# Optimization experiments

Hardware: AMD Instinct MI355X
Metric: run time of the kernel (lower is better)

## Reference

```python
import jax, jax.numpy as jnp
import numpy as np

N = 200000          # nodes
E = 6400000         # edges (avg degree 32)
IN_C, HID, OUT_C = 128, 16, 2


def gcn_conv(x, W, b, src, dst, n):
    """PyG GCNConv: out = D^{-1/2} (A + I) D^{-1/2} (x W) + b."""
    h = x @ W  # transform first (in_channels >= out_channels): [n, d_out]
    loop = jnp.arange(n)
    s = jnp.concatenate([src, loop])  # add self-loops
    d = jnp.concatenate([dst, loop])
    ew = jnp.ones(s.shape[0], x.dtype)
    deg = jax.ops.segment_sum(ew, d, num_segments=n)  # in-degree incl. self-loop
    dinv = jnp.where(deg > 0, jax.lax.rsqrt(deg), jnp.zeros((), x.dtype))
    norm = dinv[s] * dinv[d]                          # [E+n]
    msg = h[s] * norm[:, None]                        # gather + scale
    out = jax.ops.segment_sum(msg, d, num_segments=n) # scatter-add
    return out + b


def setup_inputs() -> dict:
    key = jax.random.key(0)
    k1, k2, k3, k4 = jax.random.split(key, 4)
    x = jax.random.normal(k1, (N, IN_C), dtype=jnp.float32)
    edge_index = jax.random.randint(k2, (2, E), 0, N, dtype=jnp.int64)
    # Glorot-style init like PyG GCNConv
    W1 = jax.random.normal(k3, (IN_C, HID), dtype=jnp.float32) * (1.0 / np.sqrt(IN_C))
    b1 = jnp.zeros((HID,), jnp.float32)
    W2 = jax.random.normal(k4, (HID, OUT_C), dtype=jnp.float32) * (1.0 / np.sqrt(HID))
    b2 = jnp.zeros((OUT_C,), jnp.float32)
    return {"x": x, "edge_index": edge_index, "W1": W1, "b1": b1, "W2": W2, "b2": b2}


def reference(x, edge_index, W1, b1, W2, b2):
    src, dst = edge_index[0], edge_index[1]
    h = gcn_conv(x, W1, b1, src, dst, N)
    h = jax.nn.relu(h)
    return gcn_conv(h, W2, b2, src, dst, N)
```

## Files before the change

### kernel.cpp

```cpp
#include <hip/hip_runtime.h>
#include <hip/hip_fp16.h>

#define NN   200000
#define EE   6400000
#define INC  128
#define HIDC 16
#define OUTC 2

#define TN     256
#define TSHIFT 8
#define TMASK  (TN - 1)
#define NT     782
#define CHUNK  8192
#define NBE    782
#define SCAP   9216
#define QSH    15
#define NQ     8

__global__ __launch_bounds__(1024) void k_init(int* __restrict__ gcur) {
    int t = threadIdx.x;
    if (t < NT) gcur[t] = t * SCAP;
}

__global__ __launch_bounds__(256) void k_place(const int* __restrict__ src,
                                               const int* __restrict__ dst,
                                               int* __restrict__ gcur,
                                               int* __restrict__ brec) {
    __shared__ int h[NT];
    __shared__ int lbase[NT];
    __shared__ int gofs[NT];
    __shared__ int stmp[256];
    __shared__ int lrec[CHUNK];
    __shared__ unsigned short ltid[CHUNK];

    int tid = threadIdx.x;
    int base = blockIdx.x * CHUNK;
    int nrec = EE - base; if (nrec > CHUNK) nrec = CHUNK;
    bool full = (base + CHUNK <= EE);

    for (int t = tid; t < NT; t += 256) h[t] = 0;
    __syncthreads();
    if (full) {
        for (int i = tid; i < CHUNK; i += 1024) {
            int d0 = dst[base + i];
            int d1 = dst[base + i + 256];
            int d2 = dst[base + i + 512];
            int d3 = dst[base + i + 768];
            atomicAdd(&h[d0 >> TSHIFT], 1);
            atomicAdd(&h[d1 >> TSHIFT], 1);
            atomicAdd(&h[d2 >> TSHIFT], 1);
            atomicAdd(&h[d3 >> TSHIFT], 1);
        }
    } else {
        for (int i = tid; i < nrec; i += 256)
            atomicAdd(&h[dst[base + i] >> TSHIFT], 1);
    }
    __syncthreads();

    int t0 = tid * 4;
    int c0 = (t0 + 0 < NT) ? h[t0 + 0] : 0;
    int c1 = (t0 + 1 < NT) ? h[t0 + 1] : 0;
    int c2 = (t0 + 2 < NT) ? h[t0 + 2] : 0;
    int c3 = (t0 + 3 < NT) ? h[t0 + 3] : 0;
    int s = c0 + c1 + c2 + c3;
    stmp[tid] = s;
    __syncthreads();
    for (int o = 1; o < 256; o <<= 1) {
        int u = (tid >= o) ? stmp[tid - o] : 0;
        __syncthreads();
        stmp[tid] += u;
        __syncthreads();
    }
    int run = stmp[tid] - s;
    if (t0 + 0 < NT) { lbase[t0 + 0] = run; run += c0; }
    if (t0 + 1 < NT) { lbase[t0 + 1] = run; run += c1; }
    if (t0 + 2 < NT) { lbase[t0 + 2] = run; run += c2; }
    if (t0 + 3 < NT) { lbase[t0 + 3] = run; run += c3; }
    __syncthreads();

    for (int t = tid; t < NT; t += 256) {
        int c = h[t];
        int gb = c ? atomicAdd(&gcur[t], c) : 0;
        gofs[t] = gb - lbase[t];
    }
    __syncthreads();

    if (full) {
        for (int i = tid; i < CHUNK; i += 1024) {
            int e = base + i;
            int d0 = dst[e], d1 = dst[e + 256], d2 = dst[e + 512], d3 = dst[e + 768];
            int s0 = src[e], s1 = src[e + 256], s2 = src[e + 512], s3 = src[e + 768];
            int t0_ = d0 >> TSHIFT, t1_ = d1 >> TSHIFT;
            int t2_ = d2 >> TSHIFT, t3_ = d3 >> TSHIFT;
            int p0 = atomicAdd(&lbase[t0_], 1);
            int p1 = atomicAdd(&lbase[t1_], 1);
            int p2 = atomicAdd(&lbase[t2_], 1);
            int p3 = atomicAdd(&lbase[t3_], 1);
            lrec[p0] = (s0 << 8) | (d0 & TMASK); ltid[p0] = (unsigned short)t0_;
            lrec[p1] = (s1 << 8) | (d1 & TMASK); ltid[p1] = (unsigned short)t1_;
            lrec[p2] = (s2 << 8) | (d2 & TMASK); ltid[p2] = (unsigned short)t2_;
            lrec[p3] = (s3 << 8) | (d3 & TMASK); ltid[p3] = (unsigned short)t3_;
        }
    } else {
        for (int i = tid; i < nrec; i += 256) {
            int e = base + i;
            int d = dst[e], ss = src[e];
            int tt = d >> TSHIFT;
            int p = atomicAdd(&lbase[tt], 1);
            lrec[p] = (ss << 8) | (d & TMASK); ltid[p] = (unsigned short)tt;
        }
    }
    __syncthreads();

    for (int i = tid; i < nrec; i += 256) {
        int r = lrec[i];
        int tt = ltid[i];
        brec[gofs[tt] + i] = r;
    }
}

__global__ __launch_bounds__(256) void k_sortt(int* __restrict__ brec,
                                               const int* __restrict__ gcur,
                                               int* __restrict__ nstart,
                                               int* __restrict__ ndeg) {
    __shared__ int rec[SCAP];
    __shared__ int h[TN * NQ];
    __shared__ int cur[TN * NQ];
    __shared__ int stmp[256];
    int t = blockIdx.x;
    int s0 = t * SCAP;
    int cnt = gcur[t] - s0;
    if (cnt > SCAP) cnt = SCAP;
    int tid = threadIdx.x;
    for (int k = tid; k < TN * NQ; k += 256) h[k] = 0;
    __syncthreads();
    for (int i = tid; i < cnt; i += 256) {
        int r = brec[s0 + i];
        rec[i] = r;
        unsigned q = (unsigned)(r >> 8) >> QSH;
        atomicAdd(&h[((unsigned)(r & TMASK) << 3) | q], 1);
    }
    __syncthreads();
    int k0 = tid * NQ;
    int s = 0;
#pragma unroll
    for (int j = 0; j < NQ; ++j) s += h[k0 + j];
    stmp[tid] = s;
    __syncthreads();
    for (int o = 1; o < 256; o <<= 1) {
        int u = (tid >= o) ? stmp[tid - o] : 0;
        __syncthreads();
        stmp[tid] += u;
        __syncthreads();
    }
    int run = stmp[tid] - s;
    int node = t * TN + tid;
    if (node < NN) {
        nstart[node] = s0 + run;
        ndeg[node] = s;
    }
#pragma unroll
    for (int j = 0; j < NQ; ++j) {
        cur[k0 + j] = run;
        run += h[k0 + j];
    }
    __syncthreads();
    for (int i = tid; i < cnt; i += 256) {
        int r = rec[i];
        unsigned q = (unsigned)(r >> 8) >> QSH;
        int pos = atomicAdd(&cur[((unsigned)(r & TMASK) << 3) | q], 1);
        brec[s0 + pos] = r >> 8;
    }
}

__global__ __launch_bounds__(256) void k_xw(const float* __restrict__ x,
                                            const float* __restrict__ W1,
                                            const int* __restrict__ ndeg,
                                            __half2* __restrict__ g1) {
    __shared__ float Ws[INC * HIDC];
    for (int j = threadIdx.x; j < INC * HIDC; j += 256) Ws[j] = W1[j];
    __syncthreads();
    int n = blockIdx.x * 256 + threadIdx.x;
    if (n >= NN) return;
    const float4* xr = (const float4*)(x + (size_t)n * INC);
    float acc[HIDC];
#pragma unroll
    for (int c = 0; c < HIDC; ++c) acc[c] = 0.f;
    for (int k4 = 0; k4 < INC / 4; ++k4) {
        float4 xv = xr[k4];
        const float* w0 = &Ws[(k4 * 4) * HIDC];
        float xs[4] = {xv.x, xv.y, xv.z, xv.w};
#pragma unroll
        for (int j = 0; j < 4; ++j) {
#pragma unroll
            for (int c = 0; c < HIDC; ++c) acc[c] += xs[j] * w0[j * HIDC + c];
        }
    }
    float dn = rsqrtf((float)(ndeg[n] + 1));
    union { __half2 h[8]; float4 f[2]; } u;
#pragma unroll
    for (int q = 0; q < 8; ++q)
        u.h[q] = __floats2half2_rn(dn * acc[2 * q], dn * acc[2 * q + 1]);
    float4* gp = (float4*)(g1 + (size_t)n * 8);
    gp[0] = u.f[0];
    gp[1] = u.f[1];
}

__global__ __launch_bounds__(256) void k_agg1n(const int* __restrict__ csr,
                                               const int* __restrict__ nstart,
                                               const int* __restrict__ ndeg,
                                               const __half2* __restrict__ g1,
                                               const float* __restrict__ b1,
                                               const float* __restrict__ W2,
                                               float* __restrict__ g2) {
    int lane = threadIdx.x & 7;
    int n = (blockIdx.x * 256 + threadIdx.x) >> 3;
    if (n >= NN) return;
    int rs = nstart[n];
    int deg = ndeg[n];
    int re = rs + deg;
    float dn = rsqrtf((float)(deg + 1));
    float2 s = __half22float2(g1[(size_t)n * 8 + lane]);
    float ax = s.x, ay = s.y;
    int i = rs;
    for (; i + 4 <= re; i += 4) {
        int s0 = csr[i], s1 = csr[i + 1], s2 = csr[i + 2], s3 = csr[i + 3];
        float2 f0 = __half22float2(g1[(size_t)s0 * 8 + lane]);
        float2 f1 = __half22float2(g1[(size_t)s1 * 8 + lane]);
        float2 f2 = __half22float2(g1[(size_t)s2 * 8 + lane]);
        float2 f3 = __half22float2(g1[(size_t)s3 * 8 + lane]);
        ax += f0.x + f1.x + f2.x + f3.x;
        ay += f0.y + f1.y + f2.y + f3.y;
    }
    for (; i < re; ++i) {
        float2 f = __half22float2(g1[(size_t)csr[i] * 8 + lane]);
        ax += f.x; ay += f.y;
    }
    float h0 = fmaxf(fmaf(dn, ax, b1[2 * lane]), 0.f);
    float h1 = fmaxf(fmaf(dn, ay, b1[2 * lane + 1]), 0.f);
    float p0 = h0 * W2[(2 * lane) * OUTC + 0] + h1 * W2[(2 * lane + 1) * OUTC + 0];
    float p1 = h0 * W2[(2 * lane) * OUTC + 1] + h1 * W2[(2 * lane + 1) * OUTC + 1];
#pragma unroll
    for (int o = 4; o; o >>= 1) {
        p0 += __shfl_xor(p0, o, 8);
        p1 += __shfl_xor(p1, o, 8);
    }
    if (lane == 0) {
        float2 v; v.x = dn * p0; v.y = dn * p1;
        ((float2*)g2)[n] = v;
    }
}

__global__ __launch_bounds__(256) void k_agg2n(const int* __restrict__ csr,
                                               const int* __restrict__ nstart,
                                               const int* __restrict__ ndeg,
                                               const float* __restrict__ g2,
                                               const float* __restrict__ b2,
                                               float* __restrict__ out) {
    int lane = threadIdx.x & 7;
    int n = (blockIdx.x * 256 + threadIdx.x) >> 3;
    if (n >= NN) return;
    int rs = nstart[n];
    int deg = ndeg[n];
    int re = rs + deg;
    float dn = rsqrtf((float)(deg + 1));
    float ax = 0.f, ay = 0.f;
    for (int i = rs + lane; i < re; i += 8) {
        float2 v = ((const float2*)g2)[csr[i]];
        ax += v.x; ay += v.y;
    }
#pragma unroll
    for (int o = 4; o; o >>= 1) {
        ax += __shfl_xor(ax, o, 8);
        ay += __shfl_xor(ay, o, 8);
    }
    if (lane == 0) {
        float2 g = ((const float2*)g2)[n];
        float2 o2;
        o2.x = fmaf(dn, ax + g.x, b2[0]);
        o2.y = fmaf(dn, ay + g.y, b2[1]);
        ((float2*)out)[n] = o2;
    }
}


__global__ void k_deg_f(const int* __restrict__ dst, int* __restrict__ deg) {
    int i = blockIdx.x * blockDim.x + threadIdx.x;
    if (i < EE) atomicAdd(&deg[dst[i]], 1);
}
__global__ void k_dinv_f(const int* __restrict__ deg, float* __restrict__ dinv) {
    int n = blockIdx.x * blockDim.x + threadIdx.x;
    if (n < NN) dinv[n] = rsqrtf((float)(deg[n] + 1));
}
__global__ void k_xw_f(const float* __restrict__ x, const float* __restrict__ W1,
                       const float* __restrict__ dinv, float* __restrict__ g1) {
    __shared__ float Ws[INC * HIDC];
    for (int j = threadIdx.x; j < INC * HIDC; j += 256) Ws[j] = W1[j];
    __syncthreads();
    int n = blockIdx.x * 256 + threadIdx.x;
    if (n >= NN) return;
    const float4* xr = (const float4*)(x + (size_t)n * INC);
    float acc[HIDC];
#pragma unroll
    for (int c = 0; c < HIDC; ++c) acc[c] = 0.f;
    for (int k4 = 0; k4 < INC / 4; ++k4) {
        float4 xv = xr[k4];
        const float* w0 = &Ws[(k4 * 4) * HIDC];
        float xs[4] = {xv.x, xv.y, xv.z, xv.w};
#pragma unroll
        for (int j = 0; j < 4; ++j)
#pragma unroll
            for (int c = 0; c < HIDC; ++c) acc[c] += xs[j] * w0[j * HIDC + c];
    }
    float dn = dinv[n];
#pragma unroll
    for (int c = 0; c < HIDC; ++c) g1[(size_t)n * HIDC + c] = dn * acc[c];
}
__global__ void k_scatter1_f(const int* __restrict__ src, const int* __restrict__ dst,
                             const float* __restrict__ g1, float* __restrict__ acc1) {
    int i = blockIdx.x * blockDim.x + threadIdx.x;
    if (i >= EE * 4) return;
    int e = i >> 2, q = i & 3;
    float4 v = ((const float4*)g1)[src[e] * 4 + q];
    float* p = acc1 + (size_t)dst[e] * HIDC + q * 4;
    unsafeAtomicAdd(p + 0, v.x); unsafeAtomicAdd(p + 1, v.y);
    unsafeAtomicAdd(p + 2, v.z); unsafeAtomicAdd(p + 3, v.w);
}
__global__ void k_l2_f(const float* __restrict__ g1, const float* __restrict__ acc1,
                       const float* __restrict__ dinv, const float* __restrict__ b1,
                       const float* __restrict__ W2, float* __restrict__ g2) {
    int n = blockIdx.x * blockDim.x + threadIdx.x;
    if (n >= NN) return;
    float dn = dinv[n];
    float h[HIDC];
#pragma unroll
    for (int c = 0; c < HIDC; ++c)
        h[c] = fmaxf(dn * (acc1[(size_t)n * HIDC + c] + g1[(size_t)n * HIDC + c]) + b1[c], 0.f);
    float o0 = 0.f, o1 = 0.f;
#pragma unroll
    for (int c = 0; c < HIDC; ++c) { o0 += h[c] * W2[c * 2]; o1 += h[c] * W2[c * 2 + 1]; }
    g2[(size_t)n * 2] = dn * o0; g2[(size_t)n * 2 + 1] = dn * o1;
}
__global__ void k_scatter2_f(const int* __restrict__ src, const int* __restrict__ dst,
                             const float* __restrict__ g2, float* __restrict__ acc2) {
    int e = blockIdx.x * blockDim.x + threadIdx.x;
    if (e >= EE) return;
    float2 v = ((const float2*)g2)[src[e]];
    unsafeAtomicAdd(&acc2[(size_t)dst[e] * 2], v.x);
    unsafeAtomicAdd(&acc2[(size_t)dst[e] * 2 + 1], v.y);
}
__global__ void k_final_f(const float* __restrict__ g2, const float* __restrict__ acc2,
                          const float* __restrict__ dinv, const float* __restrict__ b2,
                          float* __restrict__ out) {
    int n = blockIdx.x * blockDim.x + threadIdx.x;
    if (n >= NN) return;
    float dn = dinv[n];
    float2 a = ((const float2*)acc2)[n];
    float2 g = ((const float2*)g2)[n];
    float2 o;
    o.x = dn * (a.x + g.x) + b2[0];
    o.y = dn * (a.y + g.y) + b2[1];
    ((float2*)out)[n] = o;
}


extern "C" void kernel_launch(void* const* d_in, const int* in_sizes, int n_in,
                              void* d_out, int out_size, void* d_ws, size_t ws_size,
                              hipStream_t stream) {
    const float* x  = (const float*)d_in[0];
    const int*   ei = (const int*)d_in[1];
    const float* W1 = (const float*)d_in[2];
    const float* b1 = (const float*)d_in[3];
    const float* W2 = (const float*)d_in[4];
    const float* b2 = (const float*)d_in[5];
    float* out = (float*)d_out;

    const int* src = ei;
    const int* dst = ei + EE;
    const int B = 256;

    size_t need = ((size_t)NT + (size_t)NT * SCAP + (size_t)(NN + 1) + (size_t)NN +
                   (size_t)8 * NN + (size_t)2 * NN) * 4;
    if (ws_size >= need) {
        int* ws          = (int*)d_ws;
        int* gcur        = ws;
        int* brec        = ws + NT;
        int* nstart      = brec + (size_t)NT * SCAP;
        int* ndeg        = nstart + NN + 1;
        __half2* g1      = (__half2*)(ndeg + NN);
        float* g2        = (float*)((int*)(ndeg + NN) + (size_t)8 * NN);

        k_init  <<<1, 1024, 0, stream>>>(gcur);
        k_place <<<NBE, 256, 0, stream>>>(src, dst, gcur, brec);
        k_sortt <<<NT, 256, 0, stream>>>(brec, gcur, nstart, ndeg);
        k_xw    <<<(NN + 255) / 256, 256, 0, stream>>>(x, W1, ndeg, g1);
        k_agg1n <<<(NN * 8 + 255) / 256, 256, 0, stream>>>(brec, nstart, ndeg, g1, b1, W2, g2);
        k_agg2n <<<(NN * 8 + 255) / 256, 256, 0, stream>>>(brec, nstart, ndeg, g2, b2, out);
        return;
    }

    char* wsb = (char*)d_ws;
    int*   deg  = (int*)wsb;
    float* acc1 = (float*)(wsb + (size_t)NN * 4);
    float* acc2 = (float*)(wsb + (size_t)17 * NN * 4);
    float* dinv = (float*)(wsb + (size_t)19 * NN * 4);
    float* g1   = (float*)(wsb + (size_t)20 * NN * 4);
    float* g2   = (float*)(wsb + (size_t)36 * NN * 4);

    hipMemsetAsync(d_ws, 0, (size_t)19 * NN * 4, stream);

    int gN = (NN + B - 1) / B, gE = (EE + B - 1) / B, gE4 = (EE * 4 + B - 1) / B;
    k_deg_f     <<<gE, B, 0, stream>>>(dst, deg);
    k_dinv_f    <<<gN, B, 0, stream>>>(deg, dinv);
    k_xw_f      <<<gN, B, 0, stream>>>(x, W1, dinv, g1);
    k_scatter1_f<<<gE4, B, 0, stream>>>(src, dst, g1, acc1);
    k_l2_f      <<<gN, B, 0, stream>>>(g1, acc1, dinv, b1, W2, g2);
    k_scatter2_f<<<gE, B, 0, stream>>>(src, dst, g2, acc2);
    k_final_f   <<<gN, B, 0, stream>>>(g2, acc2, dinv, b2, out);
}
```

Before: 407.1 us.

## Replace per-node CSR aggregation with per-tile LDS atomic accumulation

The sort kernel now orders records within each 256-node tile by source-range bucket first and then by destination, keeping the packed record instead of building per-node CSR offsets. Both aggregation kernels now run one block per tile, sweeping that tile's records and accumulating into shared-memory arrays with LDS float atomics rather than walking each node's neighbor list. This removes the nstart array and the uneven per-node loops, and the source-bucket order is meant to improve gather locality. The cost is heavy LDS atomic traffic (16 atomics per edge in layer one) and a floating-point summation order that now varies between runs.

```diff
diff --git a/kernel.cpp b/kernel.cpp
--- a/kernel.cpp
+++ b/kernel.cpp
@@ -121,7 +121,6 @@
 
 __global__ __launch_bounds__(256) void k_sortt(int* __restrict__ brec,
                                                const int* __restrict__ gcur,
-                                               int* __restrict__ nstart,
                                                int* __restrict__ ndeg) {
     __shared__ int rec[SCAP];
     __shared__ int h[TN * NQ];
@@ -137,14 +136,19 @@
     for (int i = tid; i < cnt; i += 256) {
         int r = brec[s0 + i];
         rec[i] = r;
-        unsigned q = (unsigned)(r >> 8) >> QSH;
-        atomicAdd(&h[((unsigned)(r & TMASK) << 3) | q], 1);
-    }
-    __syncthreads();
-    int k0 = tid * NQ;
+        unsigned key = (((unsigned)r >> (8 + QSH)) << 8) | ((unsigned)r & TMASK);
+        atomicAdd(&h[key], 1);
+    }
+    __syncthreads();
+    int node = t * TN + tid;
+    int dsum = 0;
+#pragma unroll
+    for (int q = 0; q < NQ; ++q) dsum += h[(q << 8) | tid];
+    if (node < NN) ndeg[node] = dsum;
+    int k0 = tid * 8;
     int s = 0;
 #pragma unroll
-    for (int j = 0; j < NQ; ++j) s += h[k0 + j];
+    for (int j = 0; j < 8; ++j) s += h[k0 + j];
     stmp[tid] = s;
     __syncthreads();
     for (int o = 1; o < 256; o <<= 1) {
@@ -154,22 +158,14 @@
         __syncthreads();
     }
     int run = stmp[tid] - s;
-    int node = t * TN + tid;
-    if (node < NN) {
-        nstart[node] = s0 + run;
-        ndeg[node] = s;
-    }
-#pragma unroll
-    for (int j = 0; j < NQ; ++j) {
-        cur[k0 + j] = run;
-        run += h[k0 + j];
-    }
+#pragma unroll
+    for (int j = 0; j < 8; ++j) { cur[k0 + j] = run; run += h[k0 + j]; }
     __syncthreads();
     for (int i = tid; i < cnt; i += 256) {
         int r = rec[i];
-        unsigned q = (unsigned)(r >> 8) >> QSH;
-        int pos = atomicAdd(&cur[((unsigned)(r & TMASK) << 3) | q], 1);
-        brec[s0 + pos] = r >> 8;
+        unsigned key = (((unsigned)r >> (8 + QSH)) << 8) | ((unsigned)r & TMASK);
+        int pos = atomicAdd(&cur[key], 1);
+        brec[s0 + pos] = r;
     }
 }
 
@@ -206,79 +202,117 @@
     gp[1] = u.f[1];
 }
 
-__global__ __launch_bounds__(256) void k_agg1n(const int* __restrict__ csr,
-                                               const int* __restrict__ nstart,
+__global__ __launch_bounds__(256) void k_agg1t(const int* __restrict__ brec,
+                                               const int* __restrict__ gcur,
                                                const int* __restrict__ ndeg,
-                                               const __half2* __restrict__ g1,
+                                               const float4* __restrict__ g1,
                                                const float* __restrict__ b1,
                                                const float* __restrict__ W2,
                                                float* __restrict__ g2) {
-    int lane = threadIdx.x & 7;
-    int n = (blockIdx.x * 256 + threadIdx.x) >> 3;
-    if (n >= NN) return;
-    int rs = nstart[n];
-    int deg = ndeg[n];
-    int re = rs + deg;
-    float dn = rsqrtf((float)(deg + 1));
-    float2 s = __half22float2(g1[(size_t)n * 8 + lane]);
-    float ax = s.x, ay = s.y;
-    int i = rs;
-    for (; i + 4 <= re; i += 4) {
-        int s0 = csr[i], s1 = csr[i + 1], s2 = csr[i + 2], s3 = csr[i + 3];
-        float2 f0 = __half22float2(g1[(size_t)s0 * 8 + lane]);
-        float2 f1 = __half22float2(g1[(size_t)s1 * 8 + lane]);
-        float2 f2 = __half22float2(g1[(size_t)s2 * 8 + lane]);
-        float2 f3 = __half22float2(g1[(size_t)s3 * 8 + lane]);
-        ax += f0.x + f1.x + f2.x + f3.x;
-        ay += f0.y + f1.y + f2.y + f3.y;
-    }
-    for (; i < re; ++i) {
-        float2 f = __half22float2(g1[(size_t)csr[i] * 8 + lane]);
-        ax += f.x; ay += f.y;
-    }
-    float h0 = fmaxf(fmaf(dn, ax, b1[2 * lane]), 0.f);
-    float h1 = fmaxf(fmaf(dn, ay, b1[2 * lane + 1]), 0.f);
-    float p0 = h0 * W2[(2 * lane) * OUTC + 0] + h1 * W2[(2 * lane + 1) * OUTC + 0];
-    float p1 = h0 * W2[(2 * lane) * OUTC + 1] + h1 * W2[(2 * lane + 1) * OUTC + 1];
-#pragma unroll
-    for (int o = 4; o; o >>= 1) {
-        p0 += __shfl_xor(p0, o, 8);
-        p1 += __shfl_xor(p1, o, 8);
-    }
-    if (lane == 0) {
+    __shared__ float acc[HIDC][TN];
+    int t = blockIdx.x;
+    int tid = threadIdx.x;
+    int n = t * TN + tid;
+    union { float4 f[2]; __half2 h[8]; } us;
+    if (n < NN) { us.f[0] = g1[(size_t)n * 2]; us.f[1] = g1[(size_t)n * 2 + 1]; }
+    else        { us.f[0] = make_float4(0.f, 0.f, 0.f, 0.f);
+                  us.f[1] = make_float4(0.f, 0.f, 0.f, 0.f); }
+#pragma unroll
+    for (int q = 0; q < 8; ++q) {
+        float2 f = __half22float2(us.h[q]);
+        acc[2 * q][tid] = f.x;
+        acc[2 * q + 1][tid] = f.y;
+    }
+    __syncthreads();
+    int s0 = t * SCAP;
+    int cnt = gcur[t] - s0;
+    if (cnt > SCAP) cnt = SCAP;
+    int i = tid;
+    for (; i + 256 < cnt; i += 512) {
+        int r0 = brec[s0 + i];
+        int r1 = brec[s0 + i + 256];
+        int sA = r0 >> 8, dA = r0 & TMASK;
+        int sB = r1 >> 8, dB = r1 & TMASK;
+        union { float4 f[2]; __half2 h[8]; } uA, uB;
+        uA.f[0] = g1[(size_t)sA * 2]; uA.f[1] = g1[(size_t)sA * 2 + 1];
+        uB.f[0] = g1[(size_t)sB * 2]; uB.f[1] = g1[(size_t)sB * 2 + 1];
+#pragma unroll
+        for (int q = 0; q < 8; ++q) {
+            float2 fA = __half22float2(uA.h[q]);
+            float2 fB = __half22float2(uB.h[q]);
+            atomicAdd(&acc[2 * q][dA], fA.x);
+            atomicAdd(&acc[2 * q][dB], fB.x);
+            atomicAdd(&acc[2 * q + 1][dA], fA.y);
+            atomicAdd(&acc[2 * q + 1][dB], fB.y);
+        }
+    }
+    if (i < cnt) {
+        int r = brec[s0 + i];
+        int sA = r >> 8, dA = r & TMASK;
+        union { float4 f[2]; __half2 h[8]; } uA;
+        uA.f[0] = g1[(size_t)sA * 2]; uA.f[1] = g1[(size_t)sA * 2 + 1];
+#pragma unroll
+        for (int q = 0; q < 8; ++q) {
+            float2 f = __half22float2(uA.h[q]);
+            atomicAdd(&acc[2 * q][dA], f.x);
+            atomicAdd(&acc[2 * q + 1][dA], f.y);
+        }
+    }
+    __syncthreads();
+    if (n < NN) {
+        float dn = rsqrtf((float)(ndeg[n] + 1));
+        float p0 = 0.f, p1 = 0.f;
+#pragma unroll
+        for (int c = 0; c < HIDC; ++c) {
+            float hv = fmaxf(fmaf(dn, acc[c][tid], b1[c]), 0.f);
+            p0 = fmaf(hv, W2[c * OUTC + 0], p0);
+            p1 = fmaf(hv, W2[c * OUTC + 1], p1);
+        }
         float2 v; v.x = dn * p0; v.y = dn * p1;
         ((float2*)g2)[n] = v;
     }
 }
 
-__global__ __launch_bounds__(256) void k_agg2n(const int* __restrict__ csr,
-                                               const int* __restrict__ nstart,
+__global__ __launch_bounds__(256) void k_agg2t(const int* __restrict__ brec,
+                                               const int* __restrict__ gcur,
                                                const int* __restrict__ ndeg,
                                                const float* __restrict__ g2,
                                                const float* __restrict__ b2,
                                                float* __restrict__ out) {
-    int lane = threadIdx.x & 7;
-    int n = (blockIdx.x * 256 + threadIdx.x) >> 3;
-    if (n >= NN) return;
-    int rs = nstart[n];
-    int deg = ndeg[n];
-    int re = rs + deg;
-    float dn = rsqrtf((float)(deg + 1));
-    float ax = 0.f, ay = 0.f;
-    for (int i = rs + lane; i < re; i += 8) {
-        float2 v = ((const float2*)g2)[csr[i]];
-        ax += v.x; ay += v.y;
-    }
-#pragma unroll
-    for (int o = 4; o; o >>= 1) {
-        ax += __shfl_xor(ax, o, 8);
-        ay += __shfl_xor(ay, o, 8);
-    }
-    if (lane == 0) {
+    __shared__ float ax[TN];
+    __shared__ float ay[TN];
+    int t = blockIdx.x;
+    int tid = threadIdx.x;
+    ax[tid] = 0.f; ay[tid] = 0.f;
+    __syncthreads();
+    int s0 = t * SCAP;
+    int cnt = gcur[t] - s0;
+    if (cnt > SCAP) cnt = SCAP;
+    int i = tid;
+    for (; i + 256 < cnt; i += 512) {
+        int r0 = brec[s0 + i];
+        int r1 = brec[s0 + i + 256];
+        float2 v0 = ((const float2*)g2)[r0 >> 8];
+        float2 v1 = ((const float2*)g2)[r1 >> 8];
+        atomicAdd(&ax[r0 & TMASK], v0.x);
+        atomicAdd(&ax[r1 & TMASK], v1.x);
+        atomicAdd(&ay[r0 & TMASK], v0.y);
+        atomicAdd(&ay[r1 & TMASK], v1.y);
+    }
+    if (i < cnt) {
+        int r = brec[s0 + i];
+        float2 v = ((const float2*)g2)[r >> 8];
+        atomicAdd(&ax[r & TMASK], v.x);
+        atomicAdd(&ay[r & TMASK], v.y);
+    }
+    __syncthreads();
+    int n = t * TN + tid;
+    if (n < NN) {
+        float dn = rsqrtf((float)(ndeg[n] + 1));
         float2 g = ((const float2*)g2)[n];
         float2 o2;
-        o2.x = fmaf(dn, ax + g.x, b2[0]);
-        o2.y = fmaf(dn, ay + g.y, b2[1]);
+        o2.x = fmaf(dn, ax[tid] + g.x, b2[0]);
+        o2.y = fmaf(dn, ay[tid] + g.y, b2[1]);
         ((float2*)out)[n] = o2;
     }
 }
@@ -379,23 +413,22 @@
     const int* dst = ei + EE;
     const int B = 256;
 
-    size_t need = ((size_t)NT + (size_t)NT * SCAP + (size_t)(NN + 1) + (size_t)NN +
+    size_t need = ((size_t)NT + (size_t)NT * SCAP + (size_t)NN +
                    (size_t)8 * NN + (size_t)2 * NN) * 4;
     if (ws_size >= need) {
         int* ws          = (int*)d_ws;
         int* gcur        = ws;
         int* brec        = ws + NT;
-        int* nstart      = brec + (size_t)NT * SCAP;
-        int* ndeg        = nstart + NN + 1;
+        int* ndeg        = brec + (size_t)NT * SCAP;
         __half2* g1      = (__half2*)(ndeg + NN);
         float* g2        = (float*)((int*)(ndeg + NN) + (size_t)8 * NN);
 
         k_init  <<<1, 1024, 0, stream>>>(gcur);
         k_place <<<NBE, 256, 0, stream>>>(src, dst, gcur, brec);
-        k_sortt <<<NT, 256, 0, stream>>>(brec, gcur, nstart, ndeg);
+        k_sortt <<<NT, 256, 0, stream>>>(brec, gcur, ndeg);
         k_xw    <<<(NN + 255) / 256, 256, 0, stream>>>(x, W1, ndeg, g1);
-        k_agg1n <<<(NN * 8 + 255) / 256, 256, 0, stream>>>(brec, nstart, ndeg, g1, b1, W2, g2);
-        k_agg2n <<<(NN * 8 + 255) / 256, 256, 0, stream>>>(brec, nstart, ndeg, g2, b2, out);
+        k_agg1t <<<NT, 256, 0, stream>>>(brec, gcur, ndeg, (const float4*)g1, b1, W2, g2);
+        k_agg2t <<<NT, 256, 0, stream>>>(brec, gcur, ndeg, g2, b2, out);
         return;
     }
 
```

Measured after the change: 1.255 ms. +208.3%, slower.

## Switch aggregation kernels from 8-lanes-per-node to one thread per node

Applied to the files above, without the earlier changes.

Both aggregation kernels now assign one thread per destination node instead of an 8-lane group. Each thread loads whole 32-byte fp16 feature rows as two float4 loads per neighbour and accumulates all 16 channels in registers, which removes the cross-lane shuffle reductions. The intent is to cut shuffle overhead and issue fewer, wider gathers. In exchange, edge loops become serial per thread, the CSR index loads are no longer coalesced across lanes, degree imbalance within a wavefront causes divergence, and the 200k-thread grid offers far less parallelism to hide gather latency.

```diff
diff --git a/kernel.cpp b/kernel.cpp
--- a/kernel.cpp
+++ b/kernel.cpp
@@ -206,81 +206,94 @@
     gp[1] = u.f[1];
 }
 
-__global__ __launch_bounds__(256) void k_agg1n(const int* __restrict__ csr,
+__global__ __launch_bounds__(256) void k_agg1p(const int* __restrict__ csr,
                                                const int* __restrict__ nstart,
                                                const int* __restrict__ ndeg,
-                                               const __half2* __restrict__ g1,
+                                               const float4* __restrict__ g1,
                                                const float* __restrict__ b1,
                                                const float* __restrict__ W2,
                                                float* __restrict__ g2) {
-    int lane = threadIdx.x & 7;
-    int n = (blockIdx.x * 256 + threadIdx.x) >> 3;
+    int n = blockIdx.x * 256 + threadIdx.x;
     if (n >= NN) return;
     int rs = nstart[n];
     int deg = ndeg[n];
     int re = rs + deg;
     float dn = rsqrtf((float)(deg + 1));
-    float2 s = __half22float2(g1[(size_t)n * 8 + lane]);
-    float ax = s.x, ay = s.y;
+    float acc[HIDC];
+    {
+        union { float4 f[2]; __half2 h[8]; } u;
+        u.f[0] = g1[(size_t)n * 2]; u.f[1] = g1[(size_t)n * 2 + 1];
+#pragma unroll
+        for (int q = 0; q < 8; ++q) {
+            float2 f = __half22float2(u.h[q]);
+            acc[2 * q] = f.x; acc[2 * q + 1] = f.y;
+        }
+    }
     int i = rs;
-    for (; i + 4 <= re; i += 4) {
-        int s0 = csr[i], s1 = csr[i + 1], s2 = csr[i + 2], s3 = csr[i + 3];
-        float2 f0 = __half22float2(g1[(size_t)s0 * 8 + lane]);
-        float2 f1 = __half22float2(g1[(size_t)s1 * 8 + lane]);
-        float2 f2 = __half22float2(g1[(size_t)s2 * 8 + lane]);
-        float2 f3 = __half22float2(g1[(size_t)s3 * 8 + lane]);
-        ax += f0.x + f1.x + f2.x + f3.x;
-        ay += f0.y + f1.y + f2.y + f3.y;
-    }
-    for (; i < re; ++i) {
-        float2 f = __half22float2(g1[(size_t)csr[i] * 8 + lane]);
-        ax += f.x; ay += f.y;
-    }
-    float h0 = fmaxf(fmaf(dn, ax, b1[2 * lane]), 0.f);
-    float h1 = fmaxf(fmaf(dn, ay, b1[2 * lane + 1]), 0.f);
-    float p0 = h0 * W2[(2 * lane) * OUTC + 0] + h1 * W2[(2 * lane + 1) * OUTC + 0];
-    float p1 = h0 * W2[(2 * lane) * OUTC + 1] + h1 * W2[(2 * lane + 1) * OUTC + 1];
-#pragma unroll
-    for (int o = 4; o; o >>= 1) {
-        p0 += __shfl_xor(p0, o, 8);
-        p1 += __shfl_xor(p1, o, 8);
-    }
-    if (lane == 0) {
-        float2 v; v.x = dn * p0; v.y = dn * p1;
-        ((float2*)g2)[n] = v;
-    }
-}
-
-__global__ __launch_bounds__(256) void k_agg2n(const int* __restrict__ csr,
+    for (; i + 2 <= re; i += 2) {
+        int s0 = csr[i], s1 = csr[i + 1];
+        union { float4 f[2]; __half2 h[8]; } uA, uB;
+        uA.f[0] = g1[(size_t)s0 * 2]; uA.f[1] = g1[(size_t)s0 * 2 + 1];
+        uB.f[0] = g1[(size_t)s1 * 2]; uB.f[1] = g1[(size_t)s1 * 2 + 1];
+#pragma unroll
+        for (int q = 0; q < 8; ++q) {
+            float2 fA = __half22float2(uA.h[q]);
+            float2 fB = __half22float2(uB.h[q]);
+            acc[2 * q]     += fA.x + fB.x;
+            acc[2 * q + 1] += fA.y + fB.y;
+        }
+    }
+    if (i < re) {
+        int s0 = csr[i];
+        union { float4 f[2]; __half2 h[8]; } uA;
+        uA.f[0] = g1[(size_t)s0 * 2]; uA.f[1] = g1[(size_t)s0 * 2 + 1];
+#pragma unroll
+        for (int q = 0; q < 8; ++q) {
+            float2 f = __half22float2(uA.h[q]);
+            acc[2 * q] += f.x; acc[2 * q + 1] += f.y;
+        }
+    }
+    float p0 = 0.f, p1 = 0.f;
+#pragma unroll
+    for (int c = 0; c < HIDC; ++c) {
+        float hv = fmaxf(fmaf(dn, acc[c], b1[c]), 0.f);
+        p0 = fmaf(hv, W2[c * OUTC + 0], p0);
+        p1 = fmaf(hv, W2[c * OUTC + 1], p1);
+    }
+    float2 v; v.x = dn * p0; v.y = dn * p1;
+    ((float2*)g2)[n] = v;
+}
+
+__global__ __launch_bounds__(256) void k_agg2p(const int* __restrict__ csr,
                                                const int* __restrict__ nstart,
                                                const int* __restrict__ ndeg,
                                                const float* __restrict__ g2,
                                                const float* __restrict__ b2,
                                                float* __restrict__ out) {
-    int lane = threadIdx.x & 7;
-    int n = (blockIdx.x * 256 + threadIdx.x) >> 3;
+    int n = blockIdx.x * 256 + threadIdx.x;
     if (n >= NN) return;
     int rs = nstart[n];
     int deg = ndeg[n];
     int re = rs + deg;
     float dn = rsqrtf((float)(deg + 1));
     float ax = 0.f, ay = 0.f;
-    for (int i = rs + lane; i < re; i += 8) {
+    int i = rs;
+    for (; i + 2 <= re; i += 2) {
+        int s0 = csr[i], s1 = csr[i + 1];
+        float2 v0 = ((const float2*)g2)[s0];
+        float2 v1 = ((const float2*)g2)[s1];
+        ax += v0.x + v1.x;
+        ay += v0.y + v1.y;
+    }
+    if (i < re) {
         float2 v = ((const float2*)g2)[csr[i]];
         ax += v.x; ay += v.y;
     }
-#pragma unroll
-    for (int o = 4; o; o >>= 1) {
-        ax += __shfl_xor(ax, o, 8);
-        ay += __shfl_xor(ay, o, 8);
-    }
-    if (lane == 0) {
-        float2 g = ((const float2*)g2)[n];
-        float2 o2;
-        o2.x = fmaf(dn, ax + g.x, b2[0]);
-        o2.y = fmaf(dn, ay + g.y, b2[1]);
-        ((float2*)out)[n] = o2;
-    }
+    float2 g = ((const float2*)g2)[n];
+    float2 o2;
+    o2.x = fmaf(dn, ax + g.x, b2[0]);
+    o2.y = fmaf(dn, ay + g.y, b2[1]);
+    ((float2*)out)[n] = o2;
 }
 
 
@@ -394,8 +407,9 @@
         k_place <<<NBE, 256, 0, stream>>>(src, dst, gcur, brec);
         k_sortt <<<NT, 256, 0, stream>>>(brec, gcur, nstart, ndeg);
         k_xw    <<<(NN + 255) / 256, 256, 0, stream>>>(x, W1, ndeg, g1);
-        k_agg1n <<<(NN * 8 + 255) / 256, 256, 0, stream>>>(brec, nstart, ndeg, g1, b1, W2, g2);
-        k_agg2n <<<(NN * 8 + 255) / 256, 256, 0, stream>>>(brec, nstart, ndeg, g2, b2, out);
+        k_agg1p <<<(NN + 255) / 256, 256, 0, stream>>>(brec, nstart, ndeg,
+                                                       (const float4*)g1, b1, W2, g2);
+        k_agg2p <<<(NN + 255) / 256, 256, 0, stream>>>(brec, nstart, ndeg, g2, b2, out);
         return;
     }
 
```

Result: slower. 472.7 us (+16.1%).
